# Kernel tuning notes

Hardware: AMD Instinct MI355X
Metric: run time of the kernel (lower is better)

## Reference

```python
import jax, jax.numpy as jnp
import numpy as np

B, N = 8, 1024
NFEAT, NHID, NHEADS, NCLASS, NLAYERS = 256, 64, 8, 256, 2
ALPHA = 0.2  # LeakyReLU slope inside GAT layers
OUTER_SLOPE = 0.01  # F.leaky_relu default on concatenated heads
NEG = -9e15


def setup_inputs() -> dict:
    key = jax.random.key(0)
    ks = jax.random.split(key, 8)
    x = jax.random.normal(ks[0], (B, N, NFEAT), jnp.float32)
    adj = jax.random.randint(ks[1], (B, N, N), 0, 2).astype(jnp.int32)
    mask = jax.random.randint(ks[2], (B, N), 0, 2).astype(jnp.int32)
    W_att = (jax.random.normal(ks[3], (NHEADS, NFEAT, NHID), jnp.float32) * 0.05)
    a_att = (jax.random.normal(ks[4], (NHEADS, 2 * NHID), jnp.float32) * 0.05)
    W_out = (jax.random.normal(ks[5], (NHID * NHEADS, NCLASS), jnp.float32) * 0.05)
    a_out = (jax.random.normal(ks[6], (2 * NCLASS,), jnp.float32) * 0.05)
    ln_w = jnp.ones((NCLASS,), jnp.float32)
    ln_b = jnp.zeros((NCLASS,), jnp.float32)
    return {"x": x, "adj": adj, "mask": mask, "W_att": W_att, "a_att": a_att,
            "W_out": W_out, "a_out": a_out, "ln_w": ln_w, "ln_b": ln_b}


def _layernorm(x, w, b):
    mu = jnp.mean(x, axis=-1, keepdims=True)
    var = jnp.mean(jnp.square(x - mu), axis=-1, keepdims=True)
    return (x - mu) * jax.lax.rsqrt(var + 1e-5) * w + b


def _gat_forward(x, adj_pos, maskb, W_att, a_att, W_out, a_out, ln_w, ln_b):
    for _ in range(NLAYERS):
        # multi-head GAT layers (concat=True): e_ij = leakyrelu(f1_i + f2_j)
        h = jnp.einsum('bnf,hfo->bhno', x, W_att)            # [B,H,N,F]
        f1 = jnp.einsum('bhno,ho->bhn', h, a_att[:, :NHID])  # [B,H,N]
        f2 = jnp.einsum('bhno,ho->bhn', h, a_att[:, NHID:])
        e = jax.nn.leaky_relu(f1[:, :, :, None] + f2[:, :, None, :], ALPHA)
        att = jax.nn.softmax(jnp.where(adj_pos[:, None], e, NEG), axis=-1)
        hp = jax.nn.elu(jnp.einsum('bhnm,bhmo->bhno', att, h))
        y = jax.nn.leaky_relu(
            hp.transpose(0, 2, 1, 3).reshape(B, N, NHEADS * NHID), OUTER_SLOPE)
        # out attention layer (concat=False)
        ho = y @ W_out                                        # [B,N,C]
        g1 = ho @ a_out[:NCLASS]                              # [B,N]
        g2 = ho @ a_out[NCLASS:]
        eo = jax.nn.leaky_relu(g1[:, :, None] + g2[:, None, :], ALPHA)
        ao = jax.nn.softmax(jnp.where(adj_pos, eo, NEG), axis=-1)
        x = x + jax.nn.elu(jnp.einsum('bnm,bmo->bno', ao, ho))
        x = jnp.where(maskb, 0.0, x)
        x = _layernorm(x, ln_w, ln_b)
    return jax.nn.relu(x), jax.nn.relu(x[:, 0, :])


def reference(x, adj, mask, W_att, a_att, W_out, a_out, ln_w, ln_b):
    adj_pos = adj > 0
    maskb = (mask == 0)[:, :, None]
    return _gat_forward(x, adj_pos, maskb, W_att, a_att, W_out, a_out, ln_w, ln_b)
```

## Files before the change

### kernel.cpp

```cpp
#include <hip/hip_runtime.h>
#include <hip/hip_bf16.h>
#include <math.h>

#define BB 8
#define NN 1024
#define FF 256
#define HH 8
#define OO 64
#define CC 256

typedef __attribute__((ext_vector_type(8))) short short8;
typedef __attribute__((ext_vector_type(4))) short s16x4;
typedef __attribute__((ext_vector_type(4))) float f32x4;
typedef unsigned long long u64;

__device__ __forceinline__ short bf16s(float f) {
    __hip_bfloat16 h = __float2bfloat16(f);
    return *reinterpret_cast<short*>(&h);
}

__global__ void k_prep(const int* __restrict__ adj, const float* __restrict__ x,
                       const float* __restrict__ Wa, const float* __restrict__ Wo,
                       u64* __restrict__ adjbit, __hip_bfloat16* __restrict__ xbf,
                       __hip_bfloat16* __restrict__ WaT, __hip_bfloat16* __restrict__ WoT) {
    int bid = blockIdx.x, t = threadIdx.x;
    if (bid < 32768) {
        int i = bid * 256 + t;
        u64 m = __ballot(adj[i] > 0);
        if ((t & 63) == 0) adjbit[i >> 6] = m;
    } else if (bid < 32768 + 8192) {
        int i = (bid - 32768) * 256 + t;
        xbf[i] = __float2bfloat16(x[i]);
    } else {
        int i = (bid - 32768 - 8192) * 256 + t;
        if (i < 131072) {
            int hd = i >> 14, o = (i >> 8) & 63, f = i & 255;
            WaT[i] = __float2bfloat16(Wa[hd * 16384 + f * 64 + o]);
        } else {
            int j = i - 131072;
            int c = j >> 9, k = j & 511;
            WoT[j] = __float2bfloat16(Wo[k * 256 + c]);
        }
    }
}

__global__ void k_proj_mfma(const __hip_bfloat16* __restrict__ xbf,
                            const __hip_bfloat16* __restrict__ WaT,
                            const float* __restrict__ aatt,
                            __hip_bfloat16* __restrict__ hF,
                            float* __restrict__ f1, float* __restrict__ f2) {
    int tile = blockIdx.x, hd = blockIdx.y;
    int t = threadIdx.x, lane = t & 63, w = t >> 6;
    int r0 = tile * 64;
    int b = r0 >> 10;
    int n0 = r0 & 1023;
    int bh = b * HH + hd;
    int al = lane & 15, ah = lane >> 4;
    const __hip_bfloat16* xrow = xbf + (size_t)(r0 + w * 16 + al) * FF;
    const __hip_bfloat16* Wb = WaT + (size_t)hd * OO * FF;
    f32x4 z4 = {0.f, 0.f, 0.f, 0.f};
    f32x4 acc[4] = {z4, z4, z4, z4};
    for (int k0 = 0; k0 < FF; k0 += 32) {
        int k = k0 + ah * 8;
        short8 af = *(const short8*)&xrow[k];
#pragma unroll
        for (int cf = 0; cf < 4; ++cf) {
            int col = cf * 16 + al;
            short8 bf = *(const short8*)&Wb[(size_t)col * FF + k];
            acc[cf] = __builtin_amdgcn_mfma_f32_16x16x32_bf16(af, bf, acc[cf], 0, 0, 0);
        }
    }
    int kw = tile & 15;
    int half = w >> 1;
    int hg = (w & 1) * 2 + (ah >> 1);
    int q0 = (ah & 1) * 4;
#pragma unroll
    for (int cf = 0; cf < 4; ++cf) {
        size_t base = ((((size_t)bh * 16 + kw) * 4 + cf) * 2 + half) * 512 +
                      (hg * 16 + al) * 8 + q0;
        s16x4 v;
#pragma unroll
        for (int r = 0; r < 4; ++r) v[r] = bf16s(acc[cf][r]);
        *(s16x4*)&hF[base] = v;
    }
    int nb = n0 + w * 16 + ah * 4;
    float p1[4] = {0.f, 0.f, 0.f, 0.f}, p2[4] = {0.f, 0.f, 0.f, 0.f};
#pragma unroll
    for (int cf = 0; cf < 4; ++cf) {
        int col = cf * 16 + al;
        float a1 = aatt[hd * 2 * OO + col];
        float a2 = aatt[hd * 2 * OO + OO + col];
#pragma unroll
        for (int r = 0; r < 4; ++r) {
            p1[r] += acc[cf][r] * a1;
            p2[r] += acc[cf][r] * a2;
        }
    }
#pragma unroll
    for (int off = 1; off < 16; off <<= 1) {
#pragma unroll
        for (int r = 0; r < 4; ++r) {
            p1[r] += __shfl_xor(p1[r], off);
            p2[r] += __shfl_xor(p2[r], off);
        }
    }
    if (al == 0) {
#pragma unroll
        for (int r = 0; r < 4; ++r) {
            f1[(size_t)bh * NN + nb + r] = p1[r];
            f2[(size_t)bh * NN + nb + r] = p2[r];
        }
    }
}

__global__ void k_att_fused(const u64* __restrict__ adjbit, const float* __restrict__ f1,
                            const float* __restrict__ f2,
                            const __hip_bfloat16* __restrict__ hF,
                            __hip_bfloat16* __restrict__ ybf) {
    int orig = blockIdx.x;
    int wgid = (orig & 7) * 128 + (orig >> 3);
    int bh = wgid >> 4;
    int n0 = (wgid & 15) * 64;
    int b = bh >> 3, hd = bh & 7;
    int t = threadIdx.x, lane = t & 63, w = t >> 6;
    __shared__ float Qs[1024], Ss[1024];
    __shared__ u64 bits[64 * 17];
    const float* f2b = f2 + (size_t)bh * NN;
    for (int j = t; j < 1024; j += 256) {
        float v = f2b[j];
        Qs[j] = __expf(v);
        Ss[j] = __expf(0.2f * v);
    }
    for (int e = t; e < 1024; e += 256) {
        int rr = e >> 4, c = e & 15;
        bits[rr * 17 + c] = adjbit[((size_t)b * NN + n0 + rr) * 16 + c];
    }
    int g = lane >> 4, r = lane & 15;
    int row = w * 16 + r;
    float fl = f1[(size_t)bh * NN + n0 + row];
    float P = __expf(fl), R = __expf(0.2f * fl);
    __syncthreads();
    const __hip_bfloat16* hFb = hF + (size_t)bh * 16 * 4 * 2 * 512 + lane * 8;
    f32x4 z4 = {0.f, 0.f, 0.f, 0.f};
    f32x4 acc[4] = {z4, z4, z4, z4};
    float ps = 0.f;
    int c0 = g * 8;
#pragma unroll 2
    for (int k0 = 0; k0 < NN; k0 += 64) {
        int kw = k0 >> 6;
        u64 m = bits[row * 17 + kw];
        unsigned bl0 = (unsigned)(m >> c0) & 0xffu;
        unsigned bl1 = (unsigned)(m >> (32 + c0)) & 0xffu;
        f32x4 qa0 = *(const f32x4*)&Qs[k0 + c0];
        f32x4 qb0 = *(const f32x4*)&Qs[k0 + c0 + 4];
        f32x4 sa0 = *(const f32x4*)&Ss[k0 + c0];
        f32x4 sb0 = *(const f32x4*)&Ss[k0 + c0 + 4];
        f32x4 qa1 = *(const f32x4*)&Qs[k0 + 32 + c0];
        f32x4 qb1 = *(const f32x4*)&Qs[k0 + 32 + c0 + 4];
        f32x4 sa1 = *(const f32x4*)&Ss[k0 + 32 + c0];
        f32x4 sb1 = *(const f32x4*)&Ss[k0 + 32 + c0 + 4];
        short8 a0, a1;
#pragma unroll
        for (int e = 0; e < 4; ++e) {
            float v0 = ((bl0 >> e) & 1) ? fmaxf(P * qa0[e], R * sa0[e]) : 0.f;
            float v1 = ((bl0 >> (4 + e)) & 1) ? fmaxf(P * qb0[e], R * sb0[e]) : 0.f;
            float v2 = ((bl1 >> e) & 1) ? fmaxf(P * qa1[e], R * sa1[e]) : 0.f;
            float v3 = ((bl1 >> (4 + e)) & 1) ? fmaxf(P * qb1[e], R * sb1[e]) : 0.f;
            ps += (v0 + v1) + (v2 + v3);
            a0[e] = bf16s(v0);
            a0[4 + e] = bf16s(v1);
            a1[e] = bf16s(v2);
            a1[4 + e] = bf16s(v3);
        }
#pragma unroll
        for (int cf = 0; cf < 4; ++cf) {
            const __hip_bfloat16* blk = hFb + ((size_t)(kw * 4 + cf) * 2) * 512;
            short8 b0 = *(const short8*)&blk[0];
            short8 b1 = *(const short8*)&blk[512];
            acc[cf] = __builtin_amdgcn_mfma_f32_16x16x32_bf16(a0, b0, acc[cf], 0, 0, 0);
            acc[cf] = __builtin_amdgcn_mfma_f32_16x16x32_bf16(a1, b1, acc[cf], 0, 0, 0);
        }
    }
    ps += __shfl_xor(ps, 16);
    ps += __shfl_xor(ps, 32);
#pragma unroll
    for (int rr = 0; rr < 4; ++rr) {
        int rloc = g * 4 + rr;
        float dn = __shfl(ps, rloc);
        float ids = 1.0f / dn;
        int nrow = n0 + w * 16 + rloc;
#pragma unroll
        for (int cf = 0; cf < 4; ++cf) {
            float v = acc[cf][rr] * ids;
            float e = v > 0.f ? v : expm1f(v);
            float yv = e > 0.f ? e : 0.01f * e;
            ybf[((size_t)b * NN + nrow) * 512 + hd * OO + cf * 16 + r] =
                __float2bfloat16(yv);
        }
    }
}

__global__ void k_outproj_mfma(const __hip_bfloat16* __restrict__ ybf,
                               const __hip_bfloat16* __restrict__ WoT,
                               const float* __restrict__ ao,
                               __hip_bfloat16* __restrict__ hoF,
                               float* __restrict__ g1, float* __restrict__ g2) {
    int tile = blockIdx.x;
    int t = threadIdx.x, lane = t & 63, w = t >> 6;
    int r0 = tile * 32;
    int b = r0 >> 10;
    __shared__ __align__(16) __hip_bfloat16 As[32][520];
    __shared__ float pg1[4][32], pg2[4][32];
    for (int e = t; e < 2048; e += 256) {
        int row = e >> 6, k8 = (e & 63) * 8;
        *(short8*)&As[row][k8] = *(const short8*)&ybf[(size_t)(r0 + row) * 512 + k8];
    }
    __syncthreads();
    int al = lane & 15, ah = lane >> 4;
    f32x4 z4 = {0.f, 0.f, 0.f, 0.f};
    f32x4 acc0[4] = {z4, z4, z4, z4};
    f32x4 acc1[4] = {z4, z4, z4, z4};
    for (int k0 = 0; k0 < 512; k0 += 32) {
        int k = k0 + ah * 8;
        short8 a0 = *(const short8*)&As[al][k];
        short8 a1 = *(const short8*)&As[16 + al][k];
#pragma unroll
        for (int cf = 0; cf < 4; ++cf) {
            int col = w * 64 + cf * 16 + al;
            short8 bf = *(const short8*)&WoT[(size_t)col * 512 + k];
            acc0[cf] = __builtin_amdgcn_mfma_f32_16x16x32_bf16(a0, bf, acc0[cf], 0, 0, 0);
            acc1[cf] = __builtin_amdgcn_mfma_f32_16x16x32_bf16(a1, bf, acc1[cf], 0, 0, 0);
        }
    }
    int kw = (tile >> 1) & 15;
    int half = tile & 1;
    int hg0 = ah >> 1;
    int q0 = (ah & 1) * 4;
    float q1[8] = {0.f, 0.f, 0.f, 0.f, 0.f, 0.f, 0.f, 0.f};
    float q2[8] = {0.f, 0.f, 0.f, 0.f, 0.f, 0.f, 0.f, 0.f};
#pragma unroll
    for (int cf = 0; cf < 4; ++cf) {
        int col = w * 64 + cf * 16 + al;
        int cfB = w * 4 + cf;
        float a1v = ao[col], a2v = ao[CC + col];
        size_t base = ((((size_t)b * 16 + kw) * 16 + cfB) * 2 + half) * 512;
        s16x4 v0, v1;
#pragma unroll
        for (int r = 0; r < 4; ++r) {
            v0[r] = bf16s(acc0[cf][r]);
            v1[r] = bf16s(acc1[cf][r]);
            q1[r] += acc0[cf][r] * a1v;
            q2[r] += acc0[cf][r] * a2v;
            q1[4 + r] += acc1[cf][r] * a1v;
            q2[4 + r] += acc1[cf][r] * a2v;
        }
        *(s16x4*)&hoF[base + (hg0 * 16 + al) * 8 + q0] = v0;
        *(s16x4*)&hoF[base + ((hg0 + 2) * 16 + al) * 8 + q0] = v1;
    }
#pragma unroll
    for (int off = 1; off < 16; off <<= 1) {
#pragma unroll
        for (int j = 0; j < 8; ++j) {
            q1[j] += __shfl_xor(q1[j], off);
            q2[j] += __shfl_xor(q2[j], off);
        }
    }
    if (al == 0) {
#pragma unroll
        for (int j = 0; j < 8; ++j) {
            int row = (j >> 2) * 16 + ah * 4 + (j & 3);
            pg1[w][row] = q1[j];
            pg2[w][row] = q2[j];
        }
    }
    __syncthreads();
    if (t < 32) {
        g1[r0 + t] = pg1[0][t] + pg1[1][t] + pg1[2][t] + pg1[3][t];
        g2[r0 + t] = pg2[0][t] + pg2[1][t] + pg2[2][t] + pg2[3][t];
    }
}

__global__ void k_out_fused(const u64* __restrict__ adjbit, const float* __restrict__ g1,
                            const float* __restrict__ g2,
                            const __hip_bfloat16* __restrict__ hoF,
                            const float* __restrict__ xin, const int* __restrict__ mask,
                            const float* __restrict__ lw, const float* __restrict__ lb,
                            float* __restrict__ xout, __hip_bfloat16* __restrict__ xbfout,
                            float* __restrict__ outf, int final_) {
    int orig = blockIdx.x;
    int wgid = (orig & 7) * 64 + (orig >> 3);
    int b = wgid >> 6;
    int n0 = (wgid & 63) * 16;
    int t = threadIdx.x, lane = t & 63, w = t >> 6;
    __shared__ float Qs[1024], Ss[1024];
    __shared__ u64 bits[16 * 17];
    __shared__ float lns[4][16], lnq[4][16];
    const float* g2b = g2 + (size_t)b * NN;
    for (int j = t; j < 1024; j += 256) {
        float v = g2b[j];
        Qs[j] = __expf(v);
        Ss[j] = __expf(0.2f * v);
    }
    if (t < 256) {
        int rr = t >> 4, c = t & 15;
        bits[rr * 17 + c] = adjbit[((size_t)b * NN + n0 + rr) * 16 + c];
    }
    int g = lane >> 4, r = lane & 15;
    float gl = g1[(size_t)b * NN + n0 + r];
    float P = __expf(gl);
    float R = __expf(0.2f * gl);
    __syncthreads();
    const __hip_bfloat16* hoFb = hoF + (size_t)b * 16 * 16 * 2 * 512 + lane * 8;
    f32x4 z4 = {0.f, 0.f, 0.f, 0.f};
    f32x4 acc[4] = {z4, z4, z4, z4};
    float ps = 0.f;
    int c0 = g * 8;
#pragma unroll 2
    for (int k0 = 0; k0 < NN; k0 += 64) {
        int kw = k0 >> 6;
        u64 m = bits[r * 17 + kw];
        unsigned bl0 = (unsigned)(m >> c0) & 0xffu;
        unsigned bl1 = (unsigned)(m >> (32 + c0)) & 0xffu;
        f32x4 qa0 = *(const f32x4*)&Qs[k0 + c0];
        f32x4 qb0 = *(const f32x4*)&Qs[k0 + c0 + 4];
        f32x4 sa0 = *(const f32x4*)&Ss[k0 + c0];
        f32x4 sb0 = *(const f32x4*)&Ss[k0 + c0 + 4];
        f32x4 qa1 = *(const f32x4*)&Qs[k0 + 32 + c0];
        f32x4 qb1 = *(const f32x4*)&Qs[k0 + 32 + c0 + 4];
        f32x4 sa1 = *(const f32x4*)&Ss[k0 + 32 + c0];
        f32x4 sb1 = *(const f32x4*)&Ss[k0 + 32 + c0 + 4];
        short8 a0, a1;
#pragma unroll
        for (int e = 0; e < 4; ++e) {
            float v0 = ((bl0 >> e) & 1) ? fmaxf(P * qa0[e], R * sa0[e]) : 0.f;
            float v1 = ((bl0 >> (4 + e)) & 1) ? fmaxf(P * qb0[e], R * sb0[e]) : 0.f;
            float v2 = ((bl1 >> e) & 1) ? fmaxf(P * qa1[e], R * sa1[e]) : 0.f;
            float v3 = ((bl1 >> (4 + e)) & 1) ? fmaxf(P * qb1[e], R * sb1[e]) : 0.f;
            ps += (v0 + v1) + (v2 + v3);
            a0[e] = bf16s(v0);
            a0[4 + e] = bf16s(v1);
            a1[e] = bf16s(v2);
            a1[4 + e] = bf16s(v3);
        }
#pragma unroll
        for (int cf = 0; cf < 4; ++cf) {
            int cfB = w * 4 + cf;
            const __hip_bfloat16* blk = hoFb + ((size_t)(kw * 16 + cfB) * 2) * 512;
            short8 b0 = *(const short8*)&blk[0];
            short8 b1 = *(const short8*)&blk[512];
            acc[cf] = __builtin_amdgcn_mfma_f32_16x16x32_bf16(a0, b0, acc[cf], 0, 0, 0);
            acc[cf] = __builtin_amdgcn_mfma_f32_16x16x32_bf16(a1, b1, acc[cf], 0, 0, 0);
        }
    }
    ps += __shfl_xor(ps, 16);
    ps += __shfl_xor(ps, 32);
    float tv[4][4];
#pragma unroll
    for (int rr = 0; rr < 4; ++rr) {
        int rloc = g * 4 + rr;
        float dn = __shfl(ps, rloc);
        float ids = 1.0f / dn;
        int nrow = n0 + rloc;
        int mk = mask[b * NN + nrow];
        size_t rowo = ((size_t)b * NN + nrow) * CC;
        float s1 = 0.f, s2 = 0.f;
#pragma unroll
        for (int cf = 0; cf < 4; ++cf) {
            int col = w * 64 + cf * 16 + r;
            float v = acc[cf][rr] * ids;
            float e = v > 0.f ? v : expm1f(v);
            float tvv = (mk == 0) ? 0.f : (xin[rowo + col] + e);
            tv[rr][cf] = tvv;
            s1 += tvv;
            s2 += tvv * tvv;
        }
#pragma unroll
        for (int off = 1; off < 16; off <<= 1) {
            s1 += __shfl_xor(s1, off);
            s2 += __shfl_xor(s2, off);
        }
        if (r == 0) {
            lns[w][rloc] = s1;
            lnq[w][rloc] = s2;
        }
    }
    __syncthreads();
#pragma unroll
    for (int rr = 0; rr < 4; ++rr) {
        int rloc = g * 4 + rr;
        int nrow = n0 + rloc;
        size_t rowo = ((size_t)b * NN + nrow) * CC;
        float su = lns[0][rloc] + lns[1][rloc] + lns[2][rloc] + lns[3][rloc];
        float sq = lnq[0][rloc] + lnq[1][rloc] + lnq[2][rloc] + lnq[3][rloc];
        float mu = su * (1.0f / CC);
        float var = sq * (1.0f / CC) - mu * mu;
        float rstd = rsqrtf(var + 1e-5f);
#pragma unroll
        for (int cf = 0; cf < 4; ++cf) {
            int col = w * 64 + cf * 16 + r;
            float ln = (tv[rr][cf] - mu) * rstd * lw[col] + lb[col];
            if (final_) {
                float rv = ln > 0.f ? ln : 0.f;
                outf[rowo + col] = rv;
                if (nrow == 0) outf[(size_t)BB * NN * CC + b * CC + col] = rv;
            } else {
                xout[rowo + col] = ln;
                xbfout[rowo + col] = __float2bfloat16(ln);
            }
        }
    }
}

extern "C" void kernel_launch(void* const* d_in, const int* in_sizes, int n_in,
                              void* d_out, int out_size, void* d_ws, size_t ws_size,
                              hipStream_t stream) {
    const float* x = (const float*)d_in[0];
    const int* adj = (const int*)d_in[1];
    const int* mask = (const int*)d_in[2];
    const float* W_att = (const float*)d_in[3];
    const float* a_att = (const float*)d_in[4];
    const float* W_out = (const float*)d_in[5];
    const float* a_out = (const float*)d_in[6];
    const float* ln_w = (const float*)d_in[7];
    const float* ln_b = (const float*)d_in[8];
    float* out = (float*)d_out;

    float* ws = (float*)d_ws;
    float* xbuf = ws;
    float* xbfr = xbuf + 2097152;
    float* f1   = xbfr + 2097152;
    float* f2   = f1 + 65536;
    float* g1   = f2 + 65536;
    float* g2   = g1 + 8192;
    float* p    = g2 + 8192;
    __hip_bfloat16* xbf = (__hip_bfloat16*)xbfr;
    __hip_bfloat16* hF  = (__hip_bfloat16*)p;
    __hip_bfloat16* ybf = (__hip_bfloat16*)(p + 2097152);
    __hip_bfloat16* hoF = (__hip_bfloat16*)(p + 4194304);
    __hip_bfloat16* WaT = (__hip_bfloat16*)(p + 5242880);
    __hip_bfloat16* WoT = (__hip_bfloat16*)(p + 5308416);
    u64* adjbit = (u64*)(p + 5373952);

    k_prep<<<32768 + 8192 + 1024, 256, 0, stream>>>(adj, x, W_att, W_out,
                                                    adjbit, xbf, WaT, WoT);

    for (int layer = 0; layer < 2; ++layer) {
        const float* xin_l = layer ? xbuf : x;
        k_proj_mfma<<<dim3(128, 8), 256, 0, stream>>>(xbf, WaT, a_att, hF, f1, f2);
        k_att_fused<<<1024, 256, 0, stream>>>(adjbit, f1, f2, hF, ybf);
        k_outproj_mfma<<<256, 256, 0, stream>>>(ybf, WoT, a_out, hoF, g1, g2);
        k_out_fused<<<512, 256, 0, stream>>>(adjbit, g1, g2, hoF, xin_l, mask,
                                             ln_w, ln_b, xbuf, xbf, out, layer == 1);
    }
}
```

Before: 224.5 us.

## Use 512-thread blocks with 8 waves for output projection and output attention

The output-projection kernel moves from 32-row tiles at 256 threads to 16-row tiles at 512 threads, giving 512 blocks with an XCD-aware tile remap. Each of its 8 waves now computes 32 output columns. The fused output-attention kernel also moves to 512 threads, so each wave handles 32 columns and the layernorm partial sums are reduced across 8 waves. This raises wave-level parallelism and cuts per-thread accumulator registers, at the cost of less A-tile reuse per block and more cross-wave reduction.

Measured after the change: 208.4 us. 1.08x faster.

```diff
diff --git a/kernel.cpp b/kernel.cpp
--- a/kernel.cpp
+++ b/kernel.cpp
@@ -205,78 +205,77 @@
                                const float* __restrict__ ao,
                                __hip_bfloat16* __restrict__ hoF,
                                float* __restrict__ g1, float* __restrict__ g2) {
-    int tile = blockIdx.x;
+    int orig = blockIdx.x;
+    int tile = (orig & 7) * 64 + (orig >> 3);
     int t = threadIdx.x, lane = t & 63, w = t >> 6;
-    int r0 = tile * 32;
+    int r0 = tile * 16;
     int b = r0 >> 10;
-    __shared__ __align__(16) __hip_bfloat16 As[32][520];
-    __shared__ float pg1[4][32], pg2[4][32];
-    for (int e = t; e < 2048; e += 256) {
+    __shared__ __align__(16) __hip_bfloat16 As[16][520];
+    __shared__ float pg1[8][16], pg2[8][16];
+    for (int e = t; e < 1024; e += 512) {
         int row = e >> 6, k8 = (e & 63) * 8;
         *(short8*)&As[row][k8] = *(const short8*)&ybf[(size_t)(r0 + row) * 512 + k8];
     }
     __syncthreads();
     int al = lane & 15, ah = lane >> 4;
     f32x4 z4 = {0.f, 0.f, 0.f, 0.f};
-    f32x4 acc0[4] = {z4, z4, z4, z4};
-    f32x4 acc1[4] = {z4, z4, z4, z4};
+    f32x4 acc[2] = {z4, z4};
     for (int k0 = 0; k0 < 512; k0 += 32) {
         int k = k0 + ah * 8;
         short8 a0 = *(const short8*)&As[al][k];
-        short8 a1 = *(const short8*)&As[16 + al][k];
-#pragma unroll
-        for (int cf = 0; cf < 4; ++cf) {
-            int col = w * 64 + cf * 16 + al;
+#pragma unroll
+        for (int cf = 0; cf < 2; ++cf) {
+            int col = w * 32 + cf * 16 + al;
             short8 bf = *(const short8*)&WoT[(size_t)col * 512 + k];
-            acc0[cf] = __builtin_amdgcn_mfma_f32_16x16x32_bf16(a0, bf, acc0[cf], 0, 0, 0);
-            acc1[cf] = __builtin_amdgcn_mfma_f32_16x16x32_bf16(a1, bf, acc1[cf], 0, 0, 0);
-        }
-    }
-    int kw = (tile >> 1) & 15;
-    int half = tile & 1;
-    int hg0 = ah >> 1;
+            acc[cf] = __builtin_amdgcn_mfma_f32_16x16x32_bf16(a0, bf, acc[cf], 0, 0, 0);
+        }
+    }
+    int kw = (tile & 63) >> 2;
+    int half = (tile >> 1) & 1;
+    int hg0 = (tile & 1) * 2 + (ah >> 1);
     int q0 = (ah & 1) * 4;
-    float q1[8] = {0.f, 0.f, 0.f, 0.f, 0.f, 0.f, 0.f, 0.f};
-    float q2[8] = {0.f, 0.f, 0.f, 0.f, 0.f, 0.f, 0.f, 0.f};
-#pragma unroll
-    for (int cf = 0; cf < 4; ++cf) {
-        int col = w * 64 + cf * 16 + al;
-        int cfB = w * 4 + cf;
+    float q1[4] = {0.f, 0.f, 0.f, 0.f};
+    float q2[4] = {0.f, 0.f, 0.f, 0.f};
+#pragma unroll
+    for (int cf = 0; cf < 2; ++cf) {
+        int col = w * 32 + cf * 16 + al;
+        int cfB = w * 2 + cf;
         float a1v = ao[col], a2v = ao[CC + col];
         size_t base = ((((size_t)b * 16 + kw) * 16 + cfB) * 2 + half) * 512;
-        s16x4 v0, v1;
+        s16x4 v0;
 #pragma unroll
         for (int r = 0; r < 4; ++r) {
-            v0[r] = bf16s(acc0[cf][r]);
-            v1[r] = bf16s(acc1[cf][r]);
-            q1[r] += acc0[cf][r] * a1v;
-            q2[r] += acc0[cf][r] * a2v;
-            q1[4 + r] += acc1[cf][r] * a1v;
-            q2[4 + r] += acc1[cf][r] * a2v;
+            v0[r] = bf16s(acc[cf][r]);
+            q1[r] += acc[cf][r] * a1v;
+            q2[r] += acc[cf][r] * a2v;
         }
         *(s16x4*)&hoF[base + (hg0 * 16 + al) * 8 + q0] = v0;
-        *(s16x4*)&hoF[base + ((hg0 + 2) * 16 + al) * 8 + q0] = v1;
     }
 #pragma unroll
     for (int off = 1; off < 16; off <<= 1) {
 #pragma unroll
-        for (int j = 0; j < 8; ++j) {
+        for (int j = 0; j < 4; ++j) {
             q1[j] += __shfl_xor(q1[j], off);
             q2[j] += __shfl_xor(q2[j], off);
         }
     }
     if (al == 0) {
 #pragma unroll
-        for (int j = 0; j < 8; ++j) {
-            int row = (j >> 2) * 16 + ah * 4 + (j & 3);
-            pg1[w][row] = q1[j];
-            pg2[w][row] = q2[j];
+        for (int j = 0; j < 4; ++j) {
+            pg1[w][ah * 4 + j] = q1[j];
+            pg2[w][ah * 4 + j] = q2[j];
         }
     }
     __syncthreads();
-    if (t < 32) {
-        g1[r0 + t] = pg1[0][t] + pg1[1][t] + pg1[2][t] + pg1[3][t];
-        g2[r0 + t] = pg2[0][t] + pg2[1][t] + pg2[2][t] + pg2[3][t];
+    if (t < 16) {
+        float s1 = 0.f, s2 = 0.f;
+#pragma unroll
+        for (int ww = 0; ww < 8; ++ww) {
+            s1 += pg1[ww][t];
+            s2 += pg2[ww][t];
+        }
+        g1[r0 + t] = s1;
+        g2[r0 + t] = s2;
     }
 }
 
@@ -294,9 +293,9 @@
     int t = threadIdx.x, lane = t & 63, w = t >> 6;
     __shared__ float Qs[1024], Ss[1024];
     __shared__ u64 bits[16 * 17];
-    __shared__ float lns[4][16], lnq[4][16];
+    __shared__ float lns[8][16], lnq[8][16];
     const float* g2b = g2 + (size_t)b * NN;
-    for (int j = t; j < 1024; j += 256) {
+    for (int j = t; j < 1024; j += 512) {
         float v = g2b[j];
         Qs[j] = __expf(v);
         Ss[j] = __expf(0.2f * v);
@@ -312,7 +311,7 @@
     __syncthreads();
     const __hip_bfloat16* hoFb = hoF + (size_t)b * 16 * 16 * 2 * 512 + lane * 8;
     f32x4 z4 = {0.f, 0.f, 0.f, 0.f};
-    f32x4 acc[4] = {z4, z4, z4, z4};
+    f32x4 acc[2] = {z4, z4};
     float ps = 0.f;
     int c0 = g * 8;
 #pragma unroll 2
@@ -343,8 +342,8 @@
             a1[4 + e] = bf16s(v3);
         }
 #pragma unroll
-        for (int cf = 0; cf < 4; ++cf) {
-            int cfB = w * 4 + cf;
+        for (int cf = 0; cf < 2; ++cf) {
+            int cfB = w * 2 + cf;
             const __hip_bfloat16* blk = hoFb + ((size_t)(kw * 16 + cfB) * 2) * 512;
             short8 b0 = *(const short8*)&blk[0];
             short8 b1 = *(const short8*)&blk[512];
@@ -354,7 +353,7 @@
     }
     ps += __shfl_xor(ps, 16);
     ps += __shfl_xor(ps, 32);
-    float tv[4][4];
+    float tv[4][2];
 #pragma unroll
     for (int rr = 0; rr < 4; ++rr) {
         int rloc = g * 4 + rr;
@@ -365,8 +364,8 @@
         size_t rowo = ((size_t)b * NN + nrow) * CC;
         float s1 = 0.f, s2 = 0.f;
 #pragma unroll
-        for (int cf = 0; cf < 4; ++cf) {
-            int col = w * 64 + cf * 16 + r;
+        for (int cf = 0; cf < 2; ++cf) {
+            int col = w * 32 + cf * 16 + r;
             float v = acc[cf][rr] * ids;
             float e = v > 0.f ? v : expm1f(v);
             float tvv = (mk == 0) ? 0.f : (xin[rowo + col] + e);
@@ -390,14 +389,18 @@
         int rloc = g * 4 + rr;
         int nrow = n0 + rloc;
         size_t rowo = ((size_t)b * NN + nrow) * CC;
-        float su = lns[0][rloc] + lns[1][rloc] + lns[2][rloc] + lns[3][rloc];
-        float sq = lnq[0][rloc] + lnq[1][rloc] + lnq[2][rloc] + lnq[3][rloc];
+        float su = 0.f, sq = 0.f;
+#pragma unroll
+        for (int ww = 0; ww < 8; ++ww) {
+            su += lns[ww][rloc];
+            sq += lnq[ww][rloc];
+        }
         float mu = su * (1.0f / CC);
         float var = sq * (1.0f / CC) - mu * mu;
         float rstd = rsqrtf(var + 1e-5f);
 #pragma unroll
-        for (int cf = 0; cf < 4; ++cf) {
-            int col = w * 64 + cf * 16 + r;
+        for (int cf = 0; cf < 2; ++cf) {
+            int col = w * 32 + cf * 16 + r;
             float ln = (tv[rr][cf] - mu) * rstd * lw[col] + lb[col];
             if (final_) {
                 float rv = ln > 0.f ? ln : 0.f;
@@ -448,8 +451,8 @@
         const float* xin_l = layer ? xbuf : x;
         k_proj_mfma<<<dim3(128, 8), 256, 0, stream>>>(xbf, WaT, a_att, hF, f1, f2);
         k_att_fused<<<1024, 256, 0, stream>>>(adjbit, f1, f2, hF, ybf);
-        k_outproj_mfma<<<256, 256, 0, stream>>>(ybf, WoT, a_out, hoF, g1, g2);
-        k_out_fused<<<512, 256, 0, stream>>>(adjbit, g1, g2, hoF, xin_l, mask,
+        k_outproj_mfma<<<512, 512, 0, stream>>>(ybf, WoT, a_out, hoF, g1, g2);
+        k_out_fused<<<512, 512, 0, stream>>>(adjbit, g1, g2, hoF, xin_l, mask,
                                              ln_w, ln_b, xbuf, xbf, out, layer == 1);
     }
 }
```
